# Kernel optimization log

Measured on AMD Instinct MI355X. Metric: run time of the kernel, lower is better.

The kernel has to match this reference:

```python
import jax, jax.numpy as jnp
import numpy as np

B, TQ, T, E, H, D = 4, 2048, 2048, 2048, 16, 128
BLOCK = 4096
THETA = 10000.0


def _rope_tables():
    # LlamaRotaryEmbedding cos/sin cache of length BLOCK
    inv_freq = 1.0 / (THETA ** (jnp.arange(0, D, 2, dtype=jnp.float32) / D))
    t = jnp.arange(BLOCK, dtype=jnp.float32)
    freqs = jnp.einsum('i,j->ij', t, inv_freq)          # [BLOCK, D/2]
    emb = jnp.concatenate([freqs, freqs], axis=-1)      # [BLOCK, D]
    return jnp.cos(emb), jnp.sin(emb)


def _rotate_half(x):
    x1, x2 = jnp.split(x, 2, axis=-1)
    return jnp.concatenate([-x2, x1], axis=-1)


def setup_inputs() -> dict:
    key = jax.random.key(0)
    ks = jax.random.split(key, 9)
    s = 0.02
    x = jax.random.normal(ks[0], (B, TQ, E), dtype=jnp.float32)
    xall = jax.random.normal(ks[1], (B, T, E), dtype=jnp.float32)
    posx = jnp.sort(jax.random.randint(ks[2], (B, TQ), 0, BLOCK), axis=-1)
    posxall = jnp.sort(jax.random.randint(ks[3], (B, T), 0, BLOCK), axis=-1)
    mask = jax.random.bernoulli(ks[4], 0.15, (B, T))  # True = masked out
    Wq = jax.random.normal(ks[5], (E, H * D), dtype=jnp.float32) * s
    Wk = jax.random.normal(ks[6], (E, H * D), dtype=jnp.float32) * s
    Wv = jax.random.normal(ks[7], (E, H * D), dtype=jnp.float32) * s
    Wo = jax.random.normal(ks[8], (H * D, E), dtype=jnp.float32) * s
    return {"x": x, "xall": xall, "posx": posx, "posxall": posxall,
            "mask": mask, "Wq": Wq, "Wk": Wk, "Wv": Wv, "Wo": Wo}


def reference(x, xall, posx, posxall, mask, Wq, Wk, Wv, Wo):
    cos, sin = _rope_tables()
    # projections -> [B, H, T, D]
    q = (x @ Wq).reshape(B, TQ, H, D).transpose(0, 2, 1, 3)
    k = (xall @ Wk).reshape(B, T, H, D).transpose(0, 2, 1, 3)
    v = (xall @ Wv).reshape(B, T, H, D).transpose(0, 2, 1, 3)
    # gather-based RoPE with arbitrary per-token positions
    cosq = cos[posx][:, None]      # [B,1,TQ,D]
    sinq = sin[posx][:, None]
    cosk = cos[posxall][:, None]   # [B,1,T,D]
    sink = sin[posxall][:, None]
    q = q * cosq + _rotate_half(q) * sinq
    k = k * cosk + _rotate_half(k) * sink
    # explicit O(T^2) attention
    att = jnp.einsum('bhqd,bhkd->bhqk', q, k) * (1.0 / np.sqrt(D))
    att = jnp.where(mask[:, None, None, :], jnp.finfo(att.dtype).min, att)
    att = jax.nn.softmax(att, axis=-1)
    y = jnp.einsum('bhqk,bhkd->bhqd', att, v)
    y = y.transpose(0, 2, 1, 3).reshape(B, TQ, H * D)
    return y @ Wo
```

## Files before the change

### kernel.cpp

```cpp
#include <hip/hip_runtime.h>

typedef __bf16 bf16x8 __attribute__((ext_vector_type(8)));
typedef float f32x4 __attribute__((ext_vector_type(4)));

#define B_ 4
#define H_ 16
#define T_ 2048
#define E_ 2048
#define D_ 128

#define GLDS(g, l)                                                   \
  __builtin_amdgcn_global_load_lds(                                  \
      (const __attribute__((address_space(1))) void*)(g),            \
      (__attribute__((address_space(3))) void*)(l), 16, 0, 0)

__global__ __launch_bounds__(256) void cvt_f32_bf16(const float* __restrict__ in,
                                                    __bf16* __restrict__ out) {
  size_t i = ((size_t)blockIdx.x * 256 + threadIdx.x) * 8;
  float4 a = *(const float4*)(in + i);
  float4 b = *(const float4*)(in + i + 4);
  bf16x8 v;
  v[0] = (__bf16)a.x; v[1] = (__bf16)a.y; v[2] = (__bf16)a.z; v[3] = (__bf16)a.w;
  v[4] = (__bf16)b.x; v[5] = (__bf16)b.y; v[6] = (__bf16)b.z; v[7] = (__bf16)b.w;
  *(bf16x8*)(out + i) = v;
}

__global__ __launch_bounds__(256) void transpose_w(const float* __restrict__ W,
                                                   __bf16* __restrict__ Wt) {
  __shared__ float tile[32][33];
  int bx = blockIdx.x & 63, by = blockIdx.x >> 6;
  int tx = threadIdx.x & 31, ty = threadIdx.x >> 5;
#pragma unroll
  for (int i = 0; i < 4; i++)
    tile[ty + i * 8][tx] = W[(size_t)(by * 32 + ty + i * 8) * 2048 + bx * 32 + tx];
  __syncthreads();
#pragma unroll
  for (int i = 0; i < 4; i++)
    Wt[(size_t)(bx * 32 + ty + i * 8) * 2048 + by * 32 + tx] =
        (__bf16)tile[tx][ty + i * 8];
}

template <typename TOut>
__global__ __launch_bounds__(256, 4)
void gemm_bt(const __bf16* __restrict__ A, const __bf16* __restrict__ Bt,
             TOut* __restrict__ C, int N, int K) {
  __shared__ alignas(16) __bf16 As[128 * 64];
  __shared__ alignas(16) __bf16 Bs[128 * 64];
  const int ntiles = N >> 7;
  const int tm = blockIdx.x / ntiles, tn = blockIdx.x % ntiles;
  const int tid = threadIdx.x;
  const int wave = tid >> 6, lane = tid & 63, quad = lane >> 4, l16 = lane & 15;
  const int wrow = (wave >> 1) << 6, wcol = (wave & 1) << 6;

  const f32x4 z4 = {0.f, 0.f, 0.f, 0.f};
  f32x4 acc[4][4];
#pragma unroll
  for (int r = 0; r < 4; r++)
#pragma unroll
    for (int c = 0; c < 4; c++) acc[r][c] = z4;

  const int rlo = wave * 8 + (lane >> 3);
  const int ckc = (((lane & 7) ^ ((lane >> 3) & 7)) << 3);
  const __bf16* gA = A + ((size_t)tm * 128 + rlo) * K + ckc;
  const __bf16* gB = Bt + ((size_t)tn * 128 + rlo) * K + ckc;

  for (int k0 = 0; k0 < K; k0 += 64) {
    __syncthreads();
#pragma unroll
    for (int p = 0; p < 4; p++) {
      GLDS(gA + (size_t)(p * 32) * K + k0, &As[p * 2048 + wave * 512]);
      GLDS(gB + (size_t)(p * 32) * K + k0, &Bs[p * 2048 + wave * 512]);
    }
    __syncthreads();

#pragma unroll
    for (int sub = 0; sub < 2; sub++) {
      bf16x8 bfr[4];
#pragma unroll
      for (int c = 0; c < 4; c++) {
        int br = wcol + c * 16 + l16;
        bfr[c] = *(const bf16x8*)&Bs[br * 64 + ((((sub << 2) | quad) ^ (br & 7)) << 3)];
      }
#pragma unroll
      for (int r = 0; r < 4; r++) {
        int ar = wrow + r * 16 + l16;
        bf16x8 af =
            *(const bf16x8*)&As[ar * 64 + ((((sub << 2) | quad) ^ (ar & 7)) << 3)];
#pragma unroll
        for (int c = 0; c < 4; c++)
          acc[r][c] =
              __builtin_amdgcn_mfma_f32_16x16x32_bf16(af, bfr[c], acc[r][c], 0, 0, 0);
      }
    }
  }

  const size_t rbase = (size_t)tm * 128 + wrow + quad * 4;
  const int cbase = tn * 128 + wcol + l16;
#pragma unroll
  for (int r = 0; r < 4; r++)
#pragma unroll
    for (int c = 0; c < 4; c++)
#pragma unroll
      for (int e = 0; e < 4; e++)
        C[(rbase + r * 16 + e) * N + cbase + c * 16] = (TOut)acc[r][c][e];
}

__global__ __launch_bounds__(256) void rope_relayout(const __bf16* __restrict__ raw,
                                                     const int* __restrict__ pos,
                                                     __bf16* __restrict__ out,
                                                     float scale) {
  int row = blockIdx.x;
  int b = row >> 11, t = row & 2047;
  float p = (float)pos[row];
  for (int i = threadIdx.x; i < 1024; i += 256) {
    int h = i >> 6, d = i & 63;
    float inv = exp2f((float)d * -0.2076205059304601f);
    float ang = p * inv;
    float c = cosf(ang) * scale, s = sinf(ang) * scale;
    float q1 = (float)raw[(size_t)row * 2048 + h * 128 + d];
    float q2 = (float)raw[(size_t)row * 2048 + h * 128 + d + 64];
    size_t o = ((size_t)(b * 16 + h) * 2048 + t) * 128 + d;
    out[o] = (__bf16)(q1 * c - q2 * s);
    out[o + 64] = (__bf16)(q2 * c + q1 * s);
  }
}

__global__ __launch_bounds__(256) void vtrans(const __bf16* __restrict__ Vraw,
                                              __bf16* __restrict__ Vt) {
  __shared__ __bf16 tile[32][33];
  int dt = blockIdx.x & 3, tt = (blockIdx.x >> 2) & 63, bh = blockIdx.x >> 8;
  int b = bh >> 4, h = bh & 15;
  int tx = threadIdx.x & 31, ty = threadIdx.x >> 5;
#pragma unroll
  for (int i = 0; i < 4; i++) {
    int t = tt * 32 + ty + i * 8;
    tile[ty + i * 8][tx] = Vraw[(size_t)(b * T_ + t) * 2048 + h * 128 + dt * 32 + tx];
  }
  __syncthreads();
#pragma unroll
  for (int i = 0; i < 4; i++) {
    int d = dt * 32 + ty + i * 8;
    Vt[((size_t)bh * 128 + d) * T_ + tt * 32 + tx] = tile[tx][ty + i * 8];
  }
}

__global__ __launch_bounds__(256, 2)
void attn(const __bf16* __restrict__ Q, const __bf16* __restrict__ K,
          const __bf16* __restrict__ Vt, const int* __restrict__ mask,
          __bf16* __restrict__ Y) {
  __shared__ alignas(16) __bf16 Ks[64][136];
  __shared__ alignas(16) __bf16 Vs[128][72];
  __shared__ alignas(16) __bf16 Ps[4][32][64];

  const int qt = blockIdx.x & 15;
  const int bh = blockIdx.x >> 4;
  const int b = bh >> 4;
  const __bf16* Qb = Q + (size_t)bh * T_ * 128;
  const __bf16* Kb = K + (size_t)bh * T_ * 128;
  const __bf16* Vb = Vt + (size_t)bh * 128 * T_;
  const int* mb = mask + (size_t)b * T_;

  const int tid = threadIdx.x, wave = tid >> 6, lane = tid & 63;
  const int quad = lane >> 4, l16 = lane & 15;

  bf16x8 qf[2][4];
  {
    int qrow = qt * 128 + wave * 32 + l16;
#pragma unroll
    for (int sub = 0; sub < 2; sub++)
#pragma unroll
      for (int kc = 0; kc < 4; kc++)
        qf[sub][kc] =
            *(const bf16x8*)(Qb + (size_t)(qrow + sub * 16) * 128 + kc * 32 + quad * 8);
  }

  const f32x4 z4 = {0.f, 0.f, 0.f, 0.f};
  f32x4 o0[8], o1[8];
#pragma unroll
  for (int n = 0; n < 8; n++) { o0[n] = z4; o1[n] = z4; }
  float lacc0[4] = {0.f, 0.f, 0.f, 0.f};
  float lacc1[4] = {0.f, 0.f, 0.f, 0.f};

  for (int t0 = 0; t0 < T_; t0 += 64) {
    __syncthreads();
#pragma unroll
    for (int rr = 0; rr < 4; rr++) {
      int idx = rr * 256 + tid;
      *(uint4*)&Ks[idx >> 4][(idx & 15) << 3] =
          *(const uint4*)(Kb + (size_t)(t0 + (idx >> 4)) * 128 + ((idx & 15) << 3));
      *(uint4*)&Vs[idx >> 3][(idx & 7) << 3] =
          *(const uint4*)(Vb + (size_t)(idx >> 3) * T_ + t0 + ((idx & 7) << 3));
    }
    __syncthreads();

    f32x4 s0[4], s1[4];
#pragma unroll
    for (int c = 0; c < 4; c++) { s0[c] = z4; s1[c] = z4; }
#pragma unroll
    for (int c = 0; c < 4; c++)
#pragma unroll
      for (int kc = 0; kc < 4; kc++) {
        bf16x8 kf = *(const bf16x8*)&Ks[c * 16 + l16][kc * 32 + quad * 8];
        s0[c] = __builtin_amdgcn_mfma_f32_16x16x32_bf16(qf[0][kc], kf, s0[c], 0, 0, 0);
        s1[c] = __builtin_amdgcn_mfma_f32_16x16x32_bf16(qf[1][kc], kf, s1[c], 0, 0, 0);
      }

    int mk[4];
#pragma unroll
    for (int c = 0; c < 4; c++) mk[c] = mb[t0 + c * 16 + l16];

#pragma unroll
    for (int c = 0; c < 4; c++) {
      int pcol = (c * 16 + l16) ^ (quad << 4);
#pragma unroll
      for (int e = 0; e < 4; e++) {
        float v0 = __builtin_amdgcn_exp2f(s0[c][e]);
        float v1 = __builtin_amdgcn_exp2f(s1[c][e]);
        v0 = mk[c] ? 0.f : v0;
        v1 = mk[c] ? 0.f : v1;
        lacc0[e] += v0;
        lacc1[e] += v1;
        Ps[wave][quad * 4 + e][pcol] = (__bf16)v0;
        Ps[wave][16 + quad * 4 + e][pcol] = (__bf16)v1;
      }
    }
    __builtin_amdgcn_wave_barrier();

    const int g4 = (l16 >> 2) << 4;
#pragma unroll
    for (int kc = 0; kc < 2; kc++) {
      bf16x8 pf0 = *(const bf16x8*)&Ps[wave][l16][(kc * 32 + quad * 8) ^ g4];
      bf16x8 pf1 = *(const bf16x8*)&Ps[wave][16 + l16][(kc * 32 + quad * 8) ^ g4];
#pragma unroll
      for (int n = 0; n < 8; n++) {
        bf16x8 vf = *(const bf16x8*)&Vs[n * 16 + l16][kc * 32 + quad * 8];
        o0[n] = __builtin_amdgcn_mfma_f32_16x16x32_bf16(pf0, vf, o0[n], 0, 0, 0);
        o1[n] = __builtin_amdgcn_mfma_f32_16x16x32_bf16(pf1, vf, o1[n], 0, 0, 0);
      }
    }
    __builtin_amdgcn_wave_barrier();
  }

  const int hcol = (bh & 15) * 128;
  const size_t yrow0 = (size_t)b * T_ + qt * 128 + wave * 32 + quad * 4;
#pragma unroll
  for (int e = 0; e < 4; e++) {
    float l0 = lacc0[e], l1 = lacc1[e];
    l0 += __shfl_xor(l0, 1, 16); l1 += __shfl_xor(l1, 1, 16);
    l0 += __shfl_xor(l0, 2, 16); l1 += __shfl_xor(l1, 2, 16);
    l0 += __shfl_xor(l0, 4, 16); l1 += __shfl_xor(l1, 4, 16);
    l0 += __shfl_xor(l0, 8, 16); l1 += __shfl_xor(l1, 8, 16);
    float i0 = 1.f / l0, i1 = 1.f / l1;
#pragma unroll
    for (int n = 0; n < 8; n++) {
      Y[(yrow0 + e) * 2048 + hcol + n * 16 + l16] = (__bf16)(o0[n][e] * i0);
      Y[(yrow0 + 16 + e) * 2048 + hcol + n * 16 + l16] = (__bf16)(o1[n][e] * i1);
    }
  }
}

extern "C" void kernel_launch(void* const* d_in, const int* in_sizes, int n_in,
                              void* d_out, int out_size, void* d_ws, size_t ws_size,
                              hipStream_t stream) {
  const float* x = (const float*)d_in[0];
  const float* xall = (const float*)d_in[1];
  const int* posx = (const int*)d_in[2];
  const int* posxall = (const int*)d_in[3];
  const int* mask = (const int*)d_in[4];
  const float* Wq = (const float*)d_in[5];
  const float* Wk = (const float*)d_in[6];
  const float* Wv = (const float*)d_in[7];
  const float* Wo = (const float*)d_in[8];
  float* out = (float*)d_out;

  const size_t MB = 1024ull * 1024ull;
  if (ws_size < 192 * MB) return;
  char* ws = (char*)d_ws;
  __bf16* WqT   = (__bf16*)(ws + 0 * MB);
  __bf16* WkT   = (__bf16*)(ws + 8 * MB);
  __bf16* WvT   = (__bf16*)(ws + 16 * MB);
  __bf16* WoT   = (__bf16*)(ws + 24 * MB);
  __bf16* xb    = (__bf16*)(ws + 32 * MB);
  __bf16* xallb = (__bf16*)(ws + 64 * MB);
  __bf16* Qraw  = (__bf16*)(ws + 96 * MB);
  __bf16* Kraw  = (__bf16*)(ws + 128 * MB);
  __bf16* Vraw  = (__bf16*)(ws + 160 * MB);
  __bf16* Qr    = xb;
  __bf16* Kr    = xallb;
  __bf16* Vtp   = Qraw;
  __bf16* Y     = Kraw;

  const float QSCALE = (float)(0.08838834764831843 * 1.4426950408889634);

  cvt_f32_bf16<<<8192, 256, 0, stream>>>(x, xb);
  cvt_f32_bf16<<<8192, 256, 0, stream>>>(xall, xallb);

  transpose_w<<<4096, 256, 0, stream>>>(Wq, WqT);
  transpose_w<<<4096, 256, 0, stream>>>(Wk, WkT);
  transpose_w<<<4096, 256, 0, stream>>>(Wv, WvT);
  transpose_w<<<4096, 256, 0, stream>>>(Wo, WoT);

  gemm_bt<__bf16><<<1024, 256, 0, stream>>>(xb, WqT, Qraw, 2048, 2048);
  gemm_bt<__bf16><<<1024, 256, 0, stream>>>(xallb, WkT, Kraw, 2048, 2048);
  gemm_bt<__bf16><<<1024, 256, 0, stream>>>(xallb, WvT, Vraw, 2048, 2048);

  rope_relayout<<<8192, 256, 0, stream>>>(Qraw, posx, Qr, QSCALE);
  rope_relayout<<<8192, 256, 0, stream>>>(Kraw, posxall, Kr, 1.0f);
  vtrans<<<16384, 256, 0, stream>>>(Vraw, Vtp);

  attn<<<1024, 256, 0, stream>>>(Qr, Kr, Vtp, mask, Y);

  gemm_bt<float><<<1024, 256, 0, stream>>>(Y, WoT, out, 2048, 2048);
}
```

Baseline: 729.1 us.

## Replace projection GEMMs with 256x256 double-buffered pipelined GEMM kernel

```diff
diff --git a/kernel.cpp b/kernel.cpp
--- a/kernel.cpp
+++ b/kernel.cpp
@@ -13,6 +13,10 @@
   __builtin_amdgcn_global_load_lds(                                  \
       (const __attribute__((address_space(1))) void*)(g),            \
       (__attribute__((address_space(3))) void*)(l), 16, 0, 0)
+
+#define BAR() asm volatile("s_barrier" ::: "memory")
+
+#define MFMA16(a, b, c) __builtin_amdgcn_mfma_f32_16x16x32_bf16((a), (b), (c), 0, 0, 0)
 
 __global__ __launch_bounds__(256) void cvt_f32_bf16(const float* __restrict__ in,
                                                     __bf16* __restrict__ out) {
@@ -41,68 +45,167 @@
 }
 
 template <typename TOut>
-__global__ __launch_bounds__(256, 4)
-void gemm_bt(const __bf16* __restrict__ A, const __bf16* __restrict__ Bt,
+__global__ __launch_bounds__(512, 2)
+void gemm256(const __bf16* __restrict__ A, const __bf16* __restrict__ Bt,
              TOut* __restrict__ C, int N, int K) {
-  __shared__ alignas(16) __bf16 As[128 * 64];
-  __shared__ alignas(16) __bf16 Bs[128 * 64];
-  const int ntiles = N >> 7;
-  const int tm = blockIdx.x / ntiles, tn = blockIdx.x % ntiles;
+  __shared__ alignas(16) __bf16 As[2][256 * 64];
+  __shared__ alignas(16) __bf16 Bs[2][256 * 64];
+
+  const int nwg = gridDim.x;
+  const int wg = (blockIdx.x & 7) * (nwg >> 3) + (blockIdx.x >> 3);
+  const int ntn = N >> 8;
+  const int tm = wg / ntn, tn = wg % ntn;
+
   const int tid = threadIdx.x;
-  const int wave = tid >> 6, lane = tid & 63, quad = lane >> 4, l16 = lane & 15;
-  const int wrow = (wave >> 1) << 6, wcol = (wave & 1) << 6;
+  const int wave = tid >> 6, lane = tid & 63;
+  const int quad = lane >> 4, l16 = lane & 15;
+  const int wm = wave >> 2, wn = wave & 3;
+
+  const int srow = wave * 8 + (lane >> 3);
+  const int scol = (((lane & 7) ^ ((lane >> 3) & 7)) << 3);
+  const __bf16* gA = A + (size_t)(tm * 256 + srow) * K + scol;
+  const __bf16* gB = Bt + (size_t)(tn * 256 + srow) * K + scol;
+  const int sdst = wave * 512;
+
+#define STAGE_A(dbuf, h, U)                                                    \
+  do {                                                                         \
+    GLDS(gA + (size_t)((h)*128) * K + (size_t)(U)*64,                          \
+         &As[dbuf][(h)*128 * 64 + sdst]);                                      \
+    GLDS(gA + (size_t)((h)*128 + 64) * K + (size_t)(U)*64,                     \
+         &As[dbuf][((h)*128 + 64) * 64 + sdst]);                               \
+  } while (0)
+#define STAGE_B(dbuf, h, U)                                                    \
+  do {                                                                         \
+    GLDS(gB + (size_t)((h)*128) * K + (size_t)(U)*64,                          \
+         &Bs[dbuf][(h)*128 * 64 + sdst]);                                      \
+    GLDS(gB + (size_t)((h)*128 + 64) * K + (size_t)(U)*64,                     \
+         &Bs[dbuf][((h)*128 + 64) * 64 + sdst]);                               \
+  } while (0)
+
+  const int NT = K >> 6;
+
+  const int c0 = ((quad ^ (l16 & 7)) << 3);
+  const int c1 = (((quad ^ (l16 & 7)) ^ 4) << 3);
 
   const f32x4 z4 = {0.f, 0.f, 0.f, 0.f};
-  f32x4 acc[4][4];
-#pragma unroll
-  for (int r = 0; r < 4; r++)
-#pragma unroll
-    for (int c = 0; c < 4; c++) acc[r][c] = z4;
-
-  const int rlo = wave * 8 + (lane >> 3);
-  const int ckc = (((lane & 7) ^ ((lane >> 3) & 7)) << 3);
-  const __bf16* gA = A + ((size_t)tm * 128 + rlo) * K + ckc;
-  const __bf16* gB = Bt + ((size_t)tn * 128 + rlo) * K + ckc;
-
-  for (int k0 = 0; k0 < K; k0 += 64) {
-    __syncthreads();
-#pragma unroll
-    for (int p = 0; p < 4; p++) {
-      GLDS(gA + (size_t)(p * 32) * K + k0, &As[p * 2048 + wave * 512]);
-      GLDS(gB + (size_t)(p * 32) * K + k0, &Bs[p * 2048 + wave * 512]);
-    }
-    __syncthreads();
-
-#pragma unroll
-    for (int sub = 0; sub < 2; sub++) {
-      bf16x8 bfr[4];
-#pragma unroll
-      for (int c = 0; c < 4; c++) {
-        int br = wcol + c * 16 + l16;
-        bfr[c] = *(const bf16x8*)&Bs[br * 64 + ((((sub << 2) | quad) ^ (br & 7)) << 3)];
-      }
-#pragma unroll
-      for (int r = 0; r < 4; r++) {
-        int ar = wrow + r * 16 + l16;
-        bf16x8 af =
-            *(const bf16x8*)&As[ar * 64 + ((((sub << 2) | quad) ^ (ar & 7)) << 3)];
-#pragma unroll
-        for (int c = 0; c < 4; c++)
-          acc[r][c] =
-              __builtin_amdgcn_mfma_f32_16x16x32_bf16(af, bfr[c], acc[r][c], 0, 0, 0);
-      }
-    }
-  }
-
-  const size_t rbase = (size_t)tm * 128 + wrow + quad * 4;
-  const int cbase = tn * 128 + wcol + l16;
-#pragma unroll
-  for (int r = 0; r < 4; r++)
-#pragma unroll
-    for (int c = 0; c < 4; c++)
+  f32x4 acc[8][4];
+#pragma unroll
+  for (int m = 0; m < 8; m++)
+#pragma unroll
+    for (int n = 0; n < 4; n++) acc[m][n] = z4;
+
+  bf16x8 a[4][2], b[4][2];
+
+  STAGE_A(0, 0, 0);
+  STAGE_B(0, 0, 0);
+  STAGE_B(0, 1, 0);
+  STAGE_A(0, 1, 0);
+  STAGE_B(1, 0, 1);
+  STAGE_A(1, 0, 1);
+  STAGE_B(1, 1, 1);
+  asm volatile("s_waitcnt vmcnt(6)" ::: "memory");
+  BAR();
+
+  for (int T = 0; T < NT; ++T) {
+    const int d = T & 1;
+    const __bf16* Adb = &As[d][0];
+    const __bf16* Bdb = &Bs[d][0];
+    const bool s1 = (T + 1 < NT), s2 = (T + 2 < NT);
+
+#pragma unroll
+    for (int m = 0; m < 4; m++) {
+      const __bf16* p = &Adb[(wm * 128 + m * 16 + l16) * 64];
+      a[m][0] = *(const bf16x8*)(p + c0);
+      a[m][1] = *(const bf16x8*)(p + c1);
+    }
+#pragma unroll
+    for (int n = 0; n < 2; n++) {
+      const __bf16* p = &Bdb[(wn * 64 + n * 16 + l16) * 64];
+      b[n][0] = *(const bf16x8*)(p + c0);
+      b[n][1] = *(const bf16x8*)(p + c1);
+    }
+    if (s1) STAGE_A(d ^ 1, 1, T + 1);
+    BAR();
+    __builtin_amdgcn_s_setprio(1);
+#pragma unroll
+    for (int m = 0; m < 4; m++)
+#pragma unroll
+      for (int n = 0; n < 2; n++) {
+        acc[m][n] = MFMA16(a[m][0], b[n][0], acc[m][n]);
+        acc[m][n] = MFMA16(a[m][1], b[n][1], acc[m][n]);
+      }
+    __builtin_amdgcn_s_setprio(0);
+    BAR();
+
+#pragma unroll
+    for (int n = 2; n < 4; n++) {
+      const __bf16* p = &Bdb[(wn * 64 + n * 16 + l16) * 64];
+      b[n][0] = *(const bf16x8*)(p + c0);
+      b[n][1] = *(const bf16x8*)(p + c1);
+    }
+    BAR();
+    __builtin_amdgcn_s_setprio(1);
+#pragma unroll
+    for (int m = 0; m < 4; m++)
+#pragma unroll
+      for (int n = 2; n < 4; n++) {
+        acc[m][n] = MFMA16(a[m][0], b[n][0], acc[m][n]);
+        acc[m][n] = MFMA16(a[m][1], b[n][1], acc[m][n]);
+      }
+    __builtin_amdgcn_s_setprio(0);
+    BAR();
+
+#pragma unroll
+    for (int m = 0; m < 4; m++) {
+      const __bf16* p = &Adb[(wm * 128 + (m + 4) * 16 + l16) * 64];
+      a[m][0] = *(const bf16x8*)(p + c0);
+      a[m][1] = *(const bf16x8*)(p + c1);
+    }
+    if (s2) STAGE_B(d, 0, T + 2);
+    BAR();
+    __builtin_amdgcn_s_setprio(1);
+#pragma unroll
+    for (int m = 0; m < 4; m++)
+#pragma unroll
+      for (int n = 2; n < 4; n++) {
+        acc[m + 4][n] = MFMA16(a[m][0], b[n][0], acc[m + 4][n]);
+        acc[m + 4][n] = MFMA16(a[m][1], b[n][1], acc[m + 4][n]);
+      }
+    __builtin_amdgcn_s_setprio(0);
+    BAR();
+
+    if (s2) {
+      STAGE_A(d, 0, T + 2);
+      STAGE_B(d, 1, T + 2);
+    }
+    BAR();
+    __builtin_amdgcn_s_setprio(1);
+#pragma unroll
+    for (int m = 0; m < 4; m++)
+#pragma unroll
+      for (int n = 0; n < 2; n++) {
+        acc[m + 4][n] = MFMA16(a[m][0], b[n][0], acc[m + 4][n]);
+        acc[m + 4][n] = MFMA16(a[m][1], b[n][1], acc[m + 4][n]);
+      }
+    __builtin_amdgcn_s_setprio(0);
+    if (s2)
+      asm volatile("s_waitcnt vmcnt(6)" ::: "memory");
+    else
+      asm volatile("s_waitcnt vmcnt(0)" ::: "memory");
+    BAR();
+  }
+
+  const size_t rbase = (size_t)tm * 256 + wm * 128 + quad * 4;
+  const int cbase = tn * 256 + wn * 64 + l16;
+#pragma unroll
+  for (int m = 0; m < 8; m++)
+#pragma unroll
+    for (int n = 0; n < 4; n++)
 #pragma unroll
       for (int e = 0; e < 4; e++)
-        C[(rbase + r * 16 + e) * N + cbase + c * 16] = (TOut)acc[r][c][e];
+        C[(rbase + m * 16 + e) * N + cbase + n * 16] = (TOut)acc[m][n][e];
+#undef STAGE_A
+#undef STAGE_B
 }
 
 __global__ __launch_bounds__(256) void rope_relayout(const __bf16* __restrict__ raw,
@@ -300,9 +403,9 @@
   transpose_w<<<4096, 256, 0, stream>>>(Wv, WvT);
   transpose_w<<<4096, 256, 0, stream>>>(Wo, WoT);
 
-  gemm_bt<__bf16><<<1024, 256, 0, stream>>>(xb, WqT, Qraw, 2048, 2048);
-  gemm_bt<__bf16><<<1024, 256, 0, stream>>>(xallb, WkT, Kraw, 2048, 2048);
-  gemm_bt<__bf16><<<1024, 256, 0, stream>>>(xallb, WvT, Vraw, 2048, 2048);
+  gemm256<__bf16><<<256, 512, 0, stream>>>(xb, WqT, Qraw, 2048, 2048);
+  gemm256<__bf16><<<256, 512, 0, stream>>>(xallb, WkT, Kraw, 2048, 2048);
+  gemm256<__bf16><<<256, 512, 0, stream>>>(xallb, WvT, Vraw, 2048, 2048);
 
   rope_relayout<<<8192, 256, 0, stream>>>(Qraw, posx, Qr, QSCALE);
   rope_relayout<<<8192, 256, 0, stream>>>(Kraw, posxall, Kr, 1.0f);
@@ -310,5 +413,5 @@
 
   attn<<<1024, 256, 0, stream>>>(Qr, Kr, Vtp, mask, Y);
 
-  gemm_bt<float><<<1024, 256, 0, stream>>>(Y, WoT, out, 2048, 2048);
-}
+  gemm256<float><<<256, 512, 0, stream>>>(Y, WoT, out, 2048, 2048);
+}
```

After: 715.8 us. Within noise of the previous version (-1.8%).

## Replace projection GEMMs with 256x256 double-buffered pipelined GEMM kernel

Applied to the files above, without the earlier changes.

```diff
diff --git a/kernel.cpp b/kernel.cpp
--- a/kernel.cpp
+++ b/kernel.cpp
@@ -13,6 +13,10 @@
   __builtin_amdgcn_global_load_lds(                                  \
       (const __attribute__((address_space(1))) void*)(g),            \
       (__attribute__((address_space(3))) void*)(l), 16, 0, 0)
+
+#define BAR() __builtin_amdgcn_s_barrier()
+
+#define MFMA16(a, b, c) __builtin_amdgcn_mfma_f32_16x16x32_bf16((a), (b), (c), 0, 0, 0)
 
 __global__ __launch_bounds__(256) void cvt_f32_bf16(const float* __restrict__ in,
                                                     __bf16* __restrict__ out) {
@@ -41,68 +45,162 @@
 }
 
 template <typename TOut>
-__global__ __launch_bounds__(256, 4)
-void gemm_bt(const __bf16* __restrict__ A, const __bf16* __restrict__ Bt,
+__global__ __launch_bounds__(512, 2)
+void gemm256(const __bf16* __restrict__ A, const __bf16* __restrict__ Bt,
              TOut* __restrict__ C, int N, int K) {
-  __shared__ alignas(16) __bf16 As[128 * 64];
-  __shared__ alignas(16) __bf16 Bs[128 * 64];
-  const int ntiles = N >> 7;
-  const int tm = blockIdx.x / ntiles, tn = blockIdx.x % ntiles;
+  __shared__ alignas(16) __bf16 As0[256 * 64];
+  __shared__ alignas(16) __bf16 As1[256 * 64];
+  __shared__ alignas(16) __bf16 Bs0[256 * 64];
+  __shared__ alignas(16) __bf16 Bs1[256 * 64];
+
+  const int nwg = gridDim.x;
+  const int wg = (blockIdx.x & 7) * (nwg >> 3) + (blockIdx.x >> 3);
+  const int ntn = N >> 8;
+  const int tm = wg / ntn, tn = wg % ntn;
+
   const int tid = threadIdx.x;
-  const int wave = tid >> 6, lane = tid & 63, quad = lane >> 4, l16 = lane & 15;
-  const int wrow = (wave >> 1) << 6, wcol = (wave & 1) << 6;
+  const int wave = tid >> 6, lane = tid & 63;
+  const int quad = lane >> 4, l16 = lane & 15;
+  const int wm = wave >> 2, wn = wave & 3;
+
+  const int srow = wave * 8 + (lane >> 3);
+  const int scol = (((lane & 7) ^ ((lane >> 3) & 7)) << 3);
+  const __bf16* gA = A + (size_t)(tm * 256 + srow) * K + scol;
+  const __bf16* gB = Bt + (size_t)(tn * 256 + srow) * K + scol;
+  const int sdst = wave * 512;
+
+#define STAGE_A_TO(ARR, h, U)                                                  \
+  do {                                                                         \
+    GLDS(gA + (size_t)((h)*128) * K + (size_t)(U)*64, &ARR[(h)*8192 + sdst]);  \
+    GLDS(gA + (size_t)((h)*128 + 64) * K + (size_t)(U)*64,                     \
+         &ARR[(h)*8192 + 4096 + sdst]);                                        \
+  } while (0)
+#define STAGE_B_TO(ARR, h, U)                                                  \
+  do {                                                                         \
+    GLDS(gB + (size_t)((h)*128) * K + (size_t)(U)*64, &ARR[(h)*8192 + sdst]);  \
+    GLDS(gB + (size_t)((h)*128 + 64) * K + (size_t)(U)*64,                     \
+         &ARR[(h)*8192 + 4096 + sdst]);                                        \
+  } while (0)
+
+  const int NT = K >> 6;
+
+  const int c0 = ((quad ^ (l16 & 7)) << 3);
+  const int c1 = (((quad ^ (l16 & 7)) ^ 4) << 3);
 
   const f32x4 z4 = {0.f, 0.f, 0.f, 0.f};
-  f32x4 acc[4][4];
-#pragma unroll
-  for (int r = 0; r < 4; r++)
-#pragma unroll
-    for (int c = 0; c < 4; c++) acc[r][c] = z4;
-
-  const int rlo = wave * 8 + (lane >> 3);
-  const int ckc = (((lane & 7) ^ ((lane >> 3) & 7)) << 3);
-  const __bf16* gA = A + ((size_t)tm * 128 + rlo) * K + ckc;
-  const __bf16* gB = Bt + ((size_t)tn * 128 + rlo) * K + ckc;
-
-  for (int k0 = 0; k0 < K; k0 += 64) {
-    __syncthreads();
-#pragma unroll
-    for (int p = 0; p < 4; p++) {
-      GLDS(gA + (size_t)(p * 32) * K + k0, &As[p * 2048 + wave * 512]);
-      GLDS(gB + (size_t)(p * 32) * K + k0, &Bs[p * 2048 + wave * 512]);
-    }
-    __syncthreads();
-
-#pragma unroll
-    for (int sub = 0; sub < 2; sub++) {
-      bf16x8 bfr[4];
-#pragma unroll
-      for (int c = 0; c < 4; c++) {
-        int br = wcol + c * 16 + l16;
-        bfr[c] = *(const bf16x8*)&Bs[br * 64 + ((((sub << 2) | quad) ^ (br & 7)) << 3)];
-      }
-#pragma unroll
-      for (int r = 0; r < 4; r++) {
-        int ar = wrow + r * 16 + l16;
-        bf16x8 af =
-            *(const bf16x8*)&As[ar * 64 + ((((sub << 2) | quad) ^ (ar & 7)) << 3)];
-#pragma unroll
-        for (int c = 0; c < 4; c++)
-          acc[r][c] =
-              __builtin_amdgcn_mfma_f32_16x16x32_bf16(af, bfr[c], acc[r][c], 0, 0, 0);
-      }
-    }
-  }
-
-  const size_t rbase = (size_t)tm * 128 + wrow + quad * 4;
-  const int cbase = tn * 128 + wcol + l16;
-#pragma unroll
-  for (int r = 0; r < 4; r++)
-#pragma unroll
-    for (int c = 0; c < 4; c++)
+  f32x4 acc[8][4];
+#pragma unroll
+  for (int m = 0; m < 8; m++)
+#pragma unroll
+    for (int n = 0; n < 4; n++) acc[m][n] = z4;
+
+  bf16x8 a[4][2], b[4][2];
+
+  STAGE_A_TO(As0, 0, 0);
+  STAGE_B_TO(Bs0, 0, 0);
+  STAGE_B_TO(Bs0, 1, 0);
+  STAGE_A_TO(As0, 1, 0);
+  STAGE_B_TO(Bs1, 0, 1);
+  STAGE_A_TO(As1, 0, 1);
+  STAGE_B_TO(Bs1, 1, 1);
+  asm volatile("s_waitcnt vmcnt(6)");
+  BAR();
+
+#define KTILE(AC, BC, AN, Tc)                                                  \
+  {                                                                            \
+    const bool s1 = ((Tc) + 1 < NT), s2 = ((Tc) + 2 < NT);                     \
+                   \
+    _Pragma("unroll") for (int m = 0; m < 4; m++) {                            \
+      const __bf16* p = &AC[(wm * 128 + m * 16 + l16) * 64];                   \
+      a[m][0] = *(const bf16x8*)(p + c0);                                      \
+      a[m][1] = *(const bf16x8*)(p + c1);                                      \
+    }                                                                          \
+    _Pragma("unroll") for (int n = 0; n < 2; n++) {                            \
+      const __bf16* p = &BC[(wn * 64 + n * 16 + l16) * 64];                    \
+      b[n][0] = *(const bf16x8*)(p + c0);                                      \
+      b[n][1] = *(const bf16x8*)(p + c1);                                      \
+    }                                                                          \
+    if (s1) STAGE_A_TO(AN, 1, (Tc) + 1);                                       \
+    BAR();                                                                     \
+    asm volatile("s_waitcnt lgkmcnt(0)");                                      \
+    __builtin_amdgcn_s_setprio(1);                                             \
+    _Pragma("unroll") for (int m = 0; m < 4; m++)                              \
+        _Pragma("unroll") for (int n = 0; n < 2; n++) {                        \
+      acc[m][n] = MFMA16(a[m][0], b[n][0], acc[m][n]);                         \
+      acc[m][n] = MFMA16(a[m][1], b[n][1], acc[m][n]);                         \
+    }                                                                          \
+    __builtin_amdgcn_s_setprio(0);                                             \
+    BAR();                                                                     \
+                                                \
+    _Pragma("unroll") for (int n = 2; n < 4; n++) {                            \
+      const __bf16* p = &BC[(wn * 64 + n * 16 + l16) * 64];                    \
+      b[n][0] = *(const bf16x8*)(p + c0);                                      \
+      b[n][1] = *(const bf16x8*)(p + c1);                                      \
+    }                                                                          \
+    BAR();                                                                     \
+    asm volatile("s_waitcnt lgkmcnt(0)");                                      \
+    __builtin_amdgcn_s_setprio(1);                                             \
+    _Pragma("unroll") for (int m = 0; m < 4; m++)                              \
+        _Pragma("unroll") for (int n = 2; n < 4; n++) {                        \
+      acc[m][n] = MFMA16(a[m][0], b[n][0], acc[m][n]);                         \
+      acc[m][n] = MFMA16(a[m][1], b[n][1], acc[m][n]);                         \
+    }                                                                          \
+    __builtin_amdgcn_s_setprio(0);                                             \
+    BAR();                                                                     \
+                            \
+    _Pragma("unroll") for (int m = 0; m < 4; m++) {                            \
+      const __bf16* p = &AC[(wm * 128 + (m + 4) * 16 + l16) * 64];             \
+      a[m][0] = *(const bf16x8*)(p + c0);                                      \
+      a[m][1] = *(const bf16x8*)(p + c1);                                      \
+    }                                                                          \
+    if (s2) STAGE_B_TO(BC, 0, (Tc) + 2);                                       \
+    BAR();                                                                     \
+    asm volatile("s_waitcnt lgkmcnt(0)");                                      \
+    __builtin_amdgcn_s_setprio(1);                                             \
+    _Pragma("unroll") for (int m = 0; m < 4; m++)                              \
+        _Pragma("unroll") for (int n = 2; n < 4; n++) {                        \
+      acc[m + 4][n] = MFMA16(a[m][0], b[n][0], acc[m + 4][n]);                 \
+      acc[m + 4][n] = MFMA16(a[m][1], b[n][1], acc[m + 4][n]);                 \
+    }                                                                          \
+    __builtin_amdgcn_s_setprio(0);                                             \
+    BAR();                                                                     \
+                       \
+    if (s2) {                                                                  \
+      STAGE_A_TO(AC, 0, (Tc) + 2);                                             \
+      STAGE_B_TO(BC, 1, (Tc) + 2);                                             \
+    }                                                                          \
+    BAR();                                                                     \
+    __builtin_amdgcn_s_setprio(1);                                             \
+    _Pragma("unroll") for (int m = 0; m < 4; m++)                              \
+        _Pragma("unroll") for (int n = 0; n < 2; n++) {                        \
+      acc[m + 4][n] = MFMA16(a[m][0], b[n][0], acc[m + 4][n]);                 \
+      acc[m + 4][n] = MFMA16(a[m][1], b[n][1], acc[m + 4][n]);                 \
+    }                                                                          \
+    __builtin_amdgcn_s_setprio(0);                                             \
+    if (s2)                                                                    \
+      asm volatile("s_waitcnt vmcnt(6)");                                      \
+    else                                                                       \
+      asm volatile("s_waitcnt vmcnt(0)");                                      \
+    BAR();                                                                     \
+  }
+
+  for (int Tc = 0; Tc < NT; Tc += 2) {
+    KTILE(As0, Bs0, As1, Tc);
+    KTILE(As1, Bs1, As0, Tc + 1);
+  }
+#undef KTILE
+#undef STAGE_A_TO
+#undef STAGE_B_TO
+
+  const size_t rbase = (size_t)tm * 256 + wm * 128 + quad * 4;
+  const int cbase = tn * 256 + wn * 64 + l16;
+#pragma unroll
+  for (int m = 0; m < 8; m++)
+#pragma unroll
+    for (int n = 0; n < 4; n++)
 #pragma unroll
       for (int e = 0; e < 4; e++)
-        C[(rbase + r * 16 + e) * N + cbase + c * 16] = (TOut)acc[r][c][e];
+        C[(rbase + m * 16 + e) * N + cbase + n * 16] = (TOut)acc[m][n][e];
 }
 
 __global__ __launch_bounds__(256) void rope_relayout(const __bf16* __restrict__ raw,
@@ -300,9 +398,9 @@
   transpose_w<<<4096, 256, 0, stream>>>(Wv, WvT);
   transpose_w<<<4096, 256, 0, stream>>>(Wo, WoT);
 
-  gemm_bt<__bf16><<<1024, 256, 0, stream>>>(xb, WqT, Qraw, 2048, 2048);
-  gemm_bt<__bf16><<<1024, 256, 0, stream>>>(xallb, WkT, Kraw, 2048, 2048);
-  gemm_bt<__bf16><<<1024, 256, 0, stream>>>(xallb, WvT, Vraw, 2048, 2048);
+  gemm256<__bf16><<<256, 512, 0, stream>>>(xb, WqT, Qraw, 2048, 2048);
+  gemm256<__bf16><<<256, 512, 0, stream>>>(xallb, WkT, Kraw, 2048, 2048);
+  gemm256<__bf16><<<256, 512, 0, stream>>>(xallb, WvT, Vraw, 2048, 2048);
 
   rope_relayout<<<8192, 256, 0, stream>>>(Qraw, posx, Qr, QSCALE);
   rope_relayout<<<8192, 256, 0, stream>>>(Kraw, posxall, Kr, 1.0f);
@@ -310,5 +408,5 @@
 
   attn<<<1024, 256, 0, stream>>>(Qr, Kr, Vtp, mask, Y);
 
-  gemm_bt<float><<<1024, 256, 0, stream>>>(Y, WoT, out, 2048, 2048);
-}
+  gemm256<float><<<256, 512, 0, stream>>>(Y, WoT, out, 2048, 2048);
+}
```

New measurement: 698.3 us. 4.2% less time.
